# Optimization experiments

Measured on AMD Instinct MI355X. Metric: run time of the kernel, lower is better.

## Reference

```python
import jax, jax.numpy as jnp
import numpy as np
import math


def setup_inputs() -> dict:
    key = jax.random.key(0)
    k0, k1, k2, k3, k4 = jax.random.split(key, 5)
    in_f, out_f, nb = 512, 512, 8
    B, S = 4, 2048
    x = jax.random.normal(k0, (B, S, in_f), dtype=jnp.float32)
    # RBF params (frozen in original: basis_trainable=False)
    fan_in = in_f  # fan_in of rbf.weight.T which is (num_basis, in_features)
    bound = 1.0 / math.sqrt(fan_in)
    rbf_weight = jax.random.uniform(k1, (in_f, nb), dtype=jnp.float32,
                                    minval=-math.sqrt(3.0) * 0.33 / math.sqrt(fan_in),
                                    maxval=math.sqrt(3.0) * 0.33 / math.sqrt(fan_in))
    rbf_centers = jnp.tile(jnp.linspace(-bound, bound, nb, dtype=jnp.float32)[None, :], (in_f, 1))
    # KAN spline weight (in, nb, out); fan_in for init is in_f*nb
    fan2 = in_f * nb
    wb = math.sqrt(3.0) * 0.33 / math.sqrt(fan2)
    weight = jax.random.uniform(k2, (in_f, nb, out_f), dtype=jnp.float32, minval=-wb, maxval=wb)
    bias = jax.random.uniform(k3, (out_f,), dtype=jnp.float32,
                              minval=-1.0 / math.sqrt(fan2), maxval=1.0 / math.sqrt(fan2))
    scale_base = jax.random.uniform(k4, (in_f, out_f), dtype=jnp.float32, minval=-0.1, maxval=0.1)
    return {"x": x, "rbf_weight": rbf_weight, "rbf_centers": rbf_centers,
            "weight": weight, "bias": bias, "scale_base": scale_base}


def reference(x, rbf_weight, rbf_centers, weight, bias, scale_base):
    in_f = x.shape[-1]
    nb = rbf_weight.shape[1]
    beta = (nb / math.log2(nb)) ** 2  # get_rbf_width(2/nb, log2(nb))
    batch_shape = x.shape[:-1]
    xf = x.reshape(-1, in_f)  # (N, in)
    # RBF basis expansion: (N, in, nb)
    z = xf[:, :, None] * rbf_weight[None, :, :] - rbf_centers[None, :, :]
    phi = jnp.exp(-beta * (z * z))
    # spline contraction + base path, expressed as efficient contractions
    y = jnp.einsum('nib,ibo->no', phi, weight)
    y = y + bias + jnp.cos(xf) @ scale_base
    return y.reshape(*batch_shape, weight.shape[-1])
```

## Files before the change

kernel.cpp:

```cpp
#include <hip/hip_runtime.h>
#include <hip/hip_bf16.h>

typedef __attribute__((ext_vector_type(8))) short short8;
typedef __attribute__((ext_vector_type(4))) float f32x4;

#define IN_F 512
#define OUT_F 512
#define BK 64
#define PHI_STEPS 64
#define NSTEPS 72
#define PAN 64
#define ACH 512
#define BCH4 1024
#define NT4 4
#define BCH2 2048
#define NT2 2
#define PART_ELEMS (8192 * OUT_F)
#define C2 (-10.2591705f)

__device__ __forceinline__ short f2bf(float f) {
  unsigned u = __builtin_bit_cast(unsigned, f);
  u += 0x7fffu + ((u >> 16) & 1u);
  return (short)(u >> 16);
}

__device__ __forceinline__ void glds16(const void* g, void* l) {
  __builtin_amdgcn_global_load_lds(
      (const __attribute__((address_space(1))) unsigned int*)g,
      (__attribute__((address_space(3))) unsigned int*)l, 16, 0, 0);
}

__device__ __forceinline__ float bsrc(const float* __restrict__ w,
                                      const float* __restrict__ sb,
                                      int k, int col) {
  return (k < IN_F * 8) ? w[(size_t)k * OUT_F + col]
                        : sb[(size_t)(k - IN_F * 8) * OUT_F + col];
}

__global__ void __launch_bounds__(256) prep_b4(const float* __restrict__ w,
                                               const float* __restrict__ sb,
                                               short* __restrict__ img) {
  const int D = blockIdx.x * 256 + threadIdx.x;
  const int ci = D & (BCH4 - 1);
  const int im = D >> 10;
  const int s = im % NSTEPS;
  const int nt = im / NSTEPS;
  const int n = ci >> 3, slot = ci & 7;
  const int oct = slot ^ (n & 7);
  const int col = nt * 128 + n;
  short8 v;
#pragma unroll
  for (int j = 0; j < 8; ++j) v[j] = f2bf(bsrc(w, sb, s * 64 + oct * 8 + j, col));
  *(short8*)&img[(size_t)D * 8] = v;
}

__global__ void __launch_bounds__(256) prep_b2(const float* __restrict__ w,
                                               const float* __restrict__ sb,
                                               short* __restrict__ img) {
  const int D = blockIdx.x * 256 + threadIdx.x;
  const int ci = D & (BCH2 - 1);
  const int im = D >> 11;
  const int s = im % NSTEPS;
  const int nt = im / NSTEPS;
  const int n = ci >> 3, slot = ci & 7;
  const int oct = slot ^ (n & 7);
  const int col = nt * 256 + n;
  short8 v;
#pragma unroll
  for (int j = 0; j < 8; ++j) v[j] = f2bf(bsrc(w, sb, s * 64 + oct * 8 + j, col));
  *(short8*)&img[(size_t)D * 8] = v;
}

__global__ void __launch_bounds__(256) prep_a(const float* __restrict__ x,
                                              const float* __restrict__ rw,
                                              const float* __restrict__ rc,
                                              short* __restrict__ aimg) {
  const int D = blockIdx.x * 256 + threadIdx.x;
  const int ci = D & (ACH - 1);
  const int rest = D >> 9;
  const int s = rest % NSTEPS;
  const int pan = rest / NSTEPS;
  const int m = ci >> 3, slot = ci & 7;
  const int oct = slot ^ (m & 7);
  const int row = pan * PAN + m;
  short8 v;
  if (s < PHI_STEPS) {
    const int feat = s * 8 + oct;
    const float xv = x[(size_t)row * IN_F + feat];
    const float4 r0 = *(const float4*)(rw + feat * 8);
    const float4 r1 = *(const float4*)(rw + feat * 8 + 4);
    const float4 q0 = *(const float4*)(rc + feat * 8);
    const float4 q1 = *(const float4*)(rc + feat * 8 + 4);
    const float rwv[8] = {r0.x, r0.y, r0.z, r0.w, r1.x, r1.y, r1.z, r1.w};
    const float rcv[8] = {q0.x, q0.y, q0.z, q0.w, q1.x, q1.y, q1.z, q1.w};
#pragma unroll
    for (int j = 0; j < 8; ++j) {
      const float z = fmaf(xv, rwv[j], -rcv[j]);
      v[j] = f2bf(exp2f(C2 * z * z));
    }
  } else {
    const float* xp = x + (size_t)row * IN_F + (s - PHI_STEPS) * 64 + oct * 8;
    const float4 u0 = *(const float4*)xp, u1 = *(const float4*)(xp + 4);
    v[0] = f2bf(__cosf(u0.x)); v[1] = f2bf(__cosf(u0.y));
    v[2] = f2bf(__cosf(u0.z)); v[3] = f2bf(__cosf(u0.w));
    v[4] = f2bf(__cosf(u1.x)); v[5] = f2bf(__cosf(u1.y));
    v[6] = f2bf(__cosf(u1.z)); v[7] = f2bf(__cosf(u1.w));
  }
  *(short8*)&aimg[(size_t)D * 8] = v;
}

__global__ void __launch_bounds__(256) reduce_add(const float* __restrict__ part,
                                                  float* __restrict__ out) {
  const int n4 = PART_ELEMS / 4;
  const float4* p4 = (const float4*)part;
  float4* o4 = (float4*)out;
  for (int i = blockIdx.x * 256 + threadIdx.x; i < n4; i += gridDim.x * 256) {
    float4 a = o4[i];
    const float4 b = p4[i];
    a.x += b.x; a.y += b.y; a.z += b.z; a.w += b.w;
    o4[i] = a;
  }
}

template <int KS>
__global__ void __launch_bounds__(256, 2) kan_gemm(
    const short* __restrict__ aimg, const short* __restrict__ bimg,
    const float* __restrict__ bias, float* __restrict__ out,
    float* __restrict__ part) {
  constexpr int SPLC = NSTEPS / KS;
  __shared__ __align__(16) short A_lds[2][128 * BK];
  __shared__ __align__(16) short B_lds[2][128 * BK];

  const int t = threadIdx.x, lane = t & 63, wid = t >> 6;
  const int wm = wid >> 1, wn = wid & 1;
  const int l15 = lane & 15, kb = lane >> 4;
  const int mb = blockIdx.x, nt = blockIdx.y;
  const int ks = (KS > 1) ? blockIdx.z : 0;
  const int m0 = mb * 128, n0 = nt * 128, s0 = ks * SPLC;

  f32x4 acc[4][4];
#pragma unroll
  for (int i = 0; i < 4; ++i)
#pragma unroll
    for (int j = 0; j < 4; ++j) acc[i][j] = (f32x4){0.f, 0.f, 0.f, 0.f};

  auto stage = [&](int s, int buf) {
#pragma unroll
    for (int c = 0; c < 4; ++c) {
      const int p = c >> 1;
      const short* src = aimg +
          (((size_t)(2 * mb + p) * NSTEPS + s) * ACH + (c & 1) * 256 + wid * 64 + lane) * 8;
      glds16(src, &A_lds[buf][c * 2048 + wid * 512]);
    }
#pragma unroll
    for (int c = 0; c < 4; ++c) {
      const short* src = bimg +
          (((size_t)nt * NSTEPS + s) * BCH4 + c * 256 + wid * 64 + lane) * 8;
      glds16(src, &B_lds[buf][c * 2048 + wid * 512]);
    }
  };

  auto mfma_step = [&](int buf) {
#pragma unroll
    for (int kk = 0; kk < 2; ++kk) {
      const int sk = kk * 4 + kb;
      short8 af[4], bf[4];
#pragma unroll
      for (int mi = 0; mi < 4; ++mi) {
        const int r = wm * 64 + mi * 16 + l15;
        af[mi] = *(const short8*)&A_lds[buf][r * BK + (sk ^ (r & 7)) * 8];
      }
#pragma unroll
      for (int ni = 0; ni < 4; ++ni) {
        const int n = wn * 64 + ni * 16 + l15;
        bf[ni] = *(const short8*)&B_lds[buf][n * BK + (sk ^ (n & 7)) * 8];
      }
#pragma unroll
      for (int mi = 0; mi < 4; ++mi)
#pragma unroll
        for (int ni = 0; ni < 4; ++ni)
          acc[mi][ni] = __builtin_amdgcn_mfma_f32_16x16x32_bf16(
              af[mi], bf[ni], acc[mi][ni], 0, 0, 0);
    }
  };

  stage(s0, 0);

  for (int si = 0; si < SPLC; ++si) {
    const int c = si & 1;
    if (si + 1 < SPLC) {
      stage(s0 + si + 1, c ^ 1);
      asm volatile("s_waitcnt vmcnt(8)" ::: "memory");
    } else {
      asm volatile("s_waitcnt vmcnt(0)" ::: "memory");
    }
    __builtin_amdgcn_s_barrier();
    mfma_step(c);
    __builtin_amdgcn_s_barrier();
  }

#pragma unroll
  for (int ni = 0; ni < 4; ++ni) {
    const int col = n0 + wn * 64 + ni * 16 + l15;
    const float bb = (KS == 1 || ks == 0) ? bias[col] : 0.f;
#pragma unroll
    for (int mi = 0; mi < 4; ++mi) {
      const int rb = m0 + wm * 64 + mi * 16 + kb * 4;
#pragma unroll
      for (int r4 = 0; r4 < 4; ++r4) {
        const size_t idx = (size_t)(rb + r4) * OUT_F + col;
        if (KS == 1 || ks == 0) out[idx] = acc[mi][ni][r4] + bb;
        else                    part[idx] = acc[mi][ni][r4];
      }
    }
  }
}

template <int KS>
__global__ void __launch_bounds__(256, 2) kan_fused(
    const float* __restrict__ x, const float* __restrict__ rw,
    const float* __restrict__ rc, const float* __restrict__ bias,
    const short* __restrict__ bimg, float* __restrict__ out,
    float* __restrict__ part) {
  constexpr int SPLC = NSTEPS / KS;
  __shared__ __align__(16) short A_lds[2][64 * BK];
  __shared__ __align__(16) short B_lds[2][256 * BK];

  const int t = threadIdx.x, lane = t & 63, wid = t >> 6;
  const int l15 = lane & 15, kb = lane >> 4;
  const int m0 = blockIdx.x * 64;
  const int nt = blockIdx.y, n0 = nt * 256;
  const int ks = (KS > 1) ? blockIdx.z : 0;
  const int s0 = ks * SPLC;
  const int a_il = t & 7, a_m = t >> 3;

  f32x4 acc[4][4];
#pragma unroll
  for (int i = 0; i < 4; ++i)
#pragma unroll
    for (int j = 0; j < 4; ++j) acc[i][j] = (f32x4){0.f, 0.f, 0.f, 0.f};

  float xrA, xrB;
  float4 pr0, pr1, pc0, pc1, cA0, cA1, cB0, cB1;

  auto loadNext = [&](int s1) {
    if (s1 < PHI_STEPS) {
      const int feat = s1 * 8 + a_il;
      xrA = x[(size_t)(m0 + a_m) * IN_F + feat];
      xrB = x[(size_t)(m0 + a_m + 32) * IN_F + feat];
      pr0 = *(const float4*)(rw + feat * 8);
      pr1 = *(const float4*)(rw + feat * 8 + 4);
      pc0 = *(const float4*)(rc + feat * 8);
      pc1 = *(const float4*)(rc + feat * 8 + 4);
    } else {
      const float* xpA = x + (size_t)(m0 + a_m) * IN_F + (s1 - PHI_STEPS) * 64 + a_il * 8;
      const float* xpB = xpA + (size_t)32 * IN_F;
      cA0 = *(const float4*)xpA; cA1 = *(const float4*)(xpA + 4);
      cB0 = *(const float4*)xpB; cB1 = *(const float4*)(xpB + 4);
    }
  };

  auto writeA = [&](int s1, short* __restrict__ Ad) {
    short8 avA, avB;
    if (s1 < PHI_STEPS) {
      const float rwv[8] = {pr0.x, pr0.y, pr0.z, pr0.w, pr1.x, pr1.y, pr1.z, pr1.w};
      const float rcv[8] = {pc0.x, pc0.y, pc0.z, pc0.w, pc1.x, pc1.y, pc1.z, pc1.w};
#pragma unroll
      for (int b = 0; b < 8; ++b) {
        const float zA = fmaf(xrA, rwv[b], -rcv[b]);
        const float zB = fmaf(xrB, rwv[b], -rcv[b]);
        avA[b] = f2bf(exp2f(C2 * zA * zA));
        avB[b] = f2bf(exp2f(C2 * zB * zB));
      }
    } else {
      avA[0] = f2bf(__cosf(cA0.x)); avA[1] = f2bf(__cosf(cA0.y));
      avA[2] = f2bf(__cosf(cA0.z)); avA[3] = f2bf(__cosf(cA0.w));
      avA[4] = f2bf(__cosf(cA1.x)); avA[5] = f2bf(__cosf(cA1.y));
      avA[6] = f2bf(__cosf(cA1.z)); avA[7] = f2bf(__cosf(cA1.w));
      avB[0] = f2bf(__cosf(cB0.x)); avB[1] = f2bf(__cosf(cB0.y));
      avB[2] = f2bf(__cosf(cB0.z)); avB[3] = f2bf(__cosf(cB0.w));
      avB[4] = f2bf(__cosf(cB1.x)); avB[5] = f2bf(__cosf(cB1.y));
      avB[6] = f2bf(__cosf(cB1.z)); avB[7] = f2bf(__cosf(cB1.w));
    }
    const int mA = a_m, mB = a_m + 32;
    *(short8*)&Ad[mA * BK + (a_il ^ (mA & 7)) * 8] = avA;
    *(short8*)&Ad[mB * BK + (a_il ^ (mB & 7)) * 8] = avB;
  };

  auto stageB = [&](int s, short* __restrict__ Bd) {
    const short* src = bimg + ((size_t)(nt * NSTEPS + s) * BCH2 + t) * 8;
#pragma unroll
    for (int c = 0; c < 8; ++c)
      glds16(src + (size_t)c * 256 * 8, Bd + c * 2048 + wid * 512);
  };

  auto mfma_half = [&](const short* __restrict__ Ab, const short* __restrict__ Bb,
                       int kk) {
    const int sk = kk * 4 + kb;
    short8 af[4], bf[4];
#pragma unroll
    for (int mi = 0; mi < 4; ++mi) {
      const int r = mi * 16 + l15;
      af[mi] = *(const short8*)&Ab[r * BK + (sk ^ (r & 7)) * 8];
    }
#pragma unroll
    for (int ni = 0; ni < 4; ++ni) {
      const int n = wid * 64 + ni * 16 + l15;
      bf[ni] = *(const short8*)&Bb[n * BK + (sk ^ (n & 7)) * 8];
    }
#pragma unroll
    for (int mi = 0; mi < 4; ++mi)
#pragma unroll
      for (int ni = 0; ni < 4; ++ni)
        acc[mi][ni] = __builtin_amdgcn_mfma_f32_16x16x32_bf16(
            af[mi], bf[ni], acc[mi][ni], 0, 0, 0);
  };

  stageB(s0, B_lds[0]);
  loadNext(s0);
  writeA(s0, A_lds[0]);
  __syncthreads();

  for (int si = 0; si < SPLC; ++si) {
    const int c = si & 1;
    const int s = s0 + si;
    if (si + 1 < SPLC) { stageB(s + 1, B_lds[c ^ 1]); loadNext(s + 1); }
    mfma_half(A_lds[c], B_lds[c], 0);
    if (si + 1 < SPLC) writeA(s + 1, A_lds[c ^ 1]);
    mfma_half(A_lds[c], B_lds[c], 1);
    __syncthreads();
  }

#pragma unroll
  for (int ni = 0; ni < 4; ++ni) {
    const int col = n0 + wid * 64 + ni * 16 + l15;
    const float bb = (KS == 1 || ks == 0) ? bias[col] : 0.f;
#pragma unroll
    for (int mi = 0; mi < 4; ++mi) {
      const int rb = m0 + mi * 16 + kb * 4;
#pragma unroll
      for (int r4 = 0; r4 < 4; ++r4) {
        const size_t idx = (size_t)(rb + r4) * OUT_F + col;
        if (KS == 1 || ks == 0) out[idx] = acc[mi][ni][r4] + bb;
        else                    part[idx] = acc[mi][ni][r4];
      }
    }
  }
}

extern "C" void kernel_launch(void* const* d_in, const int* in_sizes, int n_in,
                              void* d_out, int out_size, void* d_ws, size_t ws_size,
                              hipStream_t stream) {
  const float* x    = (const float*)d_in[0];
  const float* rw   = (const float*)d_in[1];
  const float* rc   = (const float*)d_in[2];
  const float* w    = (const float*)d_in[3];
  const float* bias = (const float*)d_in[4];
  const float* sb   = (const float*)d_in[5];
  float* out = (float*)d_out;

  const int nrows = in_sizes[0] / IN_F;
  const int npan = nrows / PAN;

  const size_t b4_bytes   = (size_t)NT4 * NSTEPS * BCH4 * 16;
  const size_t b2_bytes   = (size_t)NT2 * NSTEPS * BCH2 * 16;
  const size_t aimg_bytes = (size_t)npan * NSTEPS * ACH * 16;
  const size_t part_bytes = (size_t)PART_ELEMS * sizeof(float);

  if (ws_size >= b4_bytes + aimg_bytes + part_bytes) {
    short* bimg = (short*)d_ws;
    short* aimg = (short*)((char*)d_ws + b4_bytes);
    float* part = (float*)((char*)d_ws + b4_bytes + aimg_bytes);
    prep_b4<<<NT4 * NSTEPS * BCH4 / 256, 256, 0, stream>>>(w, sb, bimg);
    prep_a<<<npan * NSTEPS * ACH / 256, 256, 0, stream>>>(x, rw, rc, aimg);
    kan_gemm<2><<<dim3(nrows / 128, 4, 2), 256, 0, stream>>>(aimg, bimg, bias, out, part);
    reduce_add<<<2048, 256, 0, stream>>>(part, out);
  } else if (ws_size >= b4_bytes + aimg_bytes) {
    short* bimg = (short*)d_ws;
    short* aimg = (short*)((char*)d_ws + b4_bytes);
    prep_b4<<<NT4 * NSTEPS * BCH4 / 256, 256, 0, stream>>>(w, sb, bimg);
    prep_a<<<npan * NSTEPS * ACH / 256, 256, 0, stream>>>(x, rw, rc, aimg);
    kan_gemm<1><<<dim3(nrows / 128, 4, 1), 256, 0, stream>>>(aimg, bimg, bias, out, nullptr);
  } else if (ws_size >= b2_bytes + part_bytes) {
    short* bimg = (short*)d_ws;
    float* part = (float*)((char*)d_ws + b2_bytes);
    prep_b2<<<NT2 * NSTEPS * BCH2 / 256, 256, 0, stream>>>(w, sb, bimg);
    kan_fused<2><<<dim3(nrows / 64, NT2, 2), 256, 0, stream>>>(x, rw, rc, bias,
                                                               bimg, out, part);
    reduce_add<<<2048, 256, 0, stream>>>(part, out);
  } else {
    short* bimg = (short*)d_ws;
    prep_b2<<<NT2 * NSTEPS * BCH2 / 256, 256, 0, stream>>>(w, sb, bimg);
    kan_fused<1><<<dim3(nrows / 64, NT2, 1), 256, 0, stream>>>(x, rw, rc, bias,
                                                               bimg, out, nullptr);
  }
}
```

Baseline: 83.28 us.

## Drop split-K GEMM, use 512-thread blocks with 4-stage LDS pipeline

Removes the split-K path and its partial-buffer write plus reduce_add kernel. The GEMM now runs 512-thread blocks (8 waves, each computing a 64x32 sub-tile) over all 72 K steps, with a 4-deep LDS prefetch ring instead of double buffering. This removes the extra reduction traffic and one launch, at the cost of halving grid parallelism (256 blocks) and using 128KB of LDS per block, which may limit occupancy to one block per CU.

```diff
diff --git a/kernel.cpp b/kernel.cpp
--- a/kernel.cpp
+++ b/kernel.cpp
@@ -122,75 +122,74 @@
   }
 }
 
-template <int KS>
-__global__ void __launch_bounds__(256, 2) kan_gemm(
+__global__ void __launch_bounds__(512, 2) kan_gemm(
     const short* __restrict__ aimg, const short* __restrict__ bimg,
-    const float* __restrict__ bias, float* __restrict__ out,
-    float* __restrict__ part) {
-  constexpr int SPLC = NSTEPS / KS;
-  __shared__ __align__(16) short A_lds[2][128 * BK];
-  __shared__ __align__(16) short B_lds[2][128 * BK];
+    const float* __restrict__ bias, float* __restrict__ out) {
+  __shared__ __align__(16) short A_lds[4][128 * BK];
+  __shared__ __align__(16) short B_lds[4][128 * BK];
 
   const int t = threadIdx.x, lane = t & 63, wid = t >> 6;
-  const int wm = wid >> 1, wn = wid & 1;
+  const int wm = wid >> 2, wn = wid & 3;
   const int l15 = lane & 15, kb = lane >> 4;
   const int mb = blockIdx.x, nt = blockIdx.y;
-  const int ks = (KS > 1) ? blockIdx.z : 0;
-  const int m0 = mb * 128, n0 = nt * 128, s0 = ks * SPLC;
-
-  f32x4 acc[4][4];
+  const int m0 = mb * 128, n0 = nt * 128;
+
+  f32x4 acc[4][2];
 #pragma unroll
   for (int i = 0; i < 4; ++i)
 #pragma unroll
-    for (int j = 0; j < 4; ++j) acc[i][j] = (f32x4){0.f, 0.f, 0.f, 0.f};
+    for (int j = 0; j < 2; ++j) acc[i][j] = (f32x4){0.f, 0.f, 0.f, 0.f};
+
+  const short* ab0 = aimg + (size_t)(2 * mb) * NSTEPS * ACH * 8;
+  const short* ab1 = aimg + (size_t)(2 * mb + 1) * NSTEPS * ACH * 8;
+  const short* bb = bimg + (size_t)nt * NSTEPS * BCH4 * 8;
 
   auto stage = [&](int s, int buf) {
-#pragma unroll
-    for (int c = 0; c < 4; ++c) {
-      const int p = c >> 1;
-      const short* src = aimg +
-          (((size_t)(2 * mb + p) * NSTEPS + s) * ACH + (c & 1) * 256 + wid * 64 + lane) * 8;
-      glds16(src, &A_lds[buf][c * 2048 + wid * 512]);
-    }
-#pragma unroll
-    for (int c = 0; c < 4; ++c) {
-      const short* src = bimg +
-          (((size_t)nt * NSTEPS + s) * BCH4 + c * 256 + wid * 64 + lane) * 8;
-      glds16(src, &B_lds[buf][c * 2048 + wid * 512]);
-    }
+    const size_t off = ((size_t)s * ACH + t) * 8;
+    glds16(ab0 + off, &A_lds[buf][wid * 512]);
+    glds16(ab1 + off, &A_lds[buf][4096 + wid * 512]);
+    const size_t boff = ((size_t)s * BCH4 + t) * 8;
+    glds16(bb + boff, &B_lds[buf][wid * 512]);
+    glds16(bb + boff + 512 * 8, &B_lds[buf][4096 + wid * 512]);
   };
 
   auto mfma_step = [&](int buf) {
 #pragma unroll
     for (int kk = 0; kk < 2; ++kk) {
       const int sk = kk * 4 + kb;
-      short8 af[4], bf[4];
+      short8 af[4], bf[2];
 #pragma unroll
       for (int mi = 0; mi < 4; ++mi) {
         const int r = wm * 64 + mi * 16 + l15;
         af[mi] = *(const short8*)&A_lds[buf][r * BK + (sk ^ (r & 7)) * 8];
       }
 #pragma unroll
-      for (int ni = 0; ni < 4; ++ni) {
-        const int n = wn * 64 + ni * 16 + l15;
+      for (int ni = 0; ni < 2; ++ni) {
+        const int n = wn * 32 + ni * 16 + l15;
         bf[ni] = *(const short8*)&B_lds[buf][n * BK + (sk ^ (n & 7)) * 8];
       }
 #pragma unroll
       for (int mi = 0; mi < 4; ++mi)
 #pragma unroll
-        for (int ni = 0; ni < 4; ++ni)
+        for (int ni = 0; ni < 2; ++ni)
           acc[mi][ni] = __builtin_amdgcn_mfma_f32_16x16x32_bf16(
               af[mi], bf[ni], acc[mi][ni], 0, 0, 0);
     }
   };
 
-  stage(s0, 0);
-
-  for (int si = 0; si < SPLC; ++si) {
-    const int c = si & 1;
-    if (si + 1 < SPLC) {
-      stage(s0 + si + 1, c ^ 1);
+  stage(0, 0);
+  stage(1, 1);
+  stage(2, 2);
+
+  for (int si = 0; si < NSTEPS; ++si) {
+    const int c = si & 3;
+    if (si + 3 < NSTEPS) {
+      stage(si + 3, (si + 3) & 3);
+      asm volatile("s_waitcnt vmcnt(12)" ::: "memory");
+    } else if (si + 2 < NSTEPS) {
       asm volatile("s_waitcnt vmcnt(8)" ::: "memory");
+    } else if (si + 1 < NSTEPS) {
+      asm volatile("s_waitcnt vmcnt(4)" ::: "memory");
     } else {
       asm volatile("s_waitcnt vmcnt(0)" ::: "memory");
     }
@@ -200,18 +199,15 @@
   }
 
 #pragma unroll
-  for (int ni = 0; ni < 4; ++ni) {
-    const int col = n0 + wn * 64 + ni * 16 + l15;
-    const float bb = (KS == 1 || ks == 0) ? bias[col] : 0.f;
+  for (int ni = 0; ni < 2; ++ni) {
+    const int col = n0 + wn * 32 + ni * 16 + l15;
+    const float bb_ = bias[col];
 #pragma unroll
     for (int mi = 0; mi < 4; ++mi) {
       const int rb = m0 + wm * 64 + mi * 16 + kb * 4;
 #pragma unroll
-      for (int r4 = 0; r4 < 4; ++r4) {
-        const size_t idx = (size_t)(rb + r4) * OUT_F + col;
-        if (KS == 1 || ks == 0) out[idx] = acc[mi][ni][r4] + bb;
-        else                    part[idx] = acc[mi][ni][r4];
-      }
+      for (int r4 = 0; r4 < 4; ++r4)
+        out[(size_t)(rb + r4) * OUT_F + col] = acc[mi][ni][r4] + bb_;
     }
   }
 }
@@ -367,20 +363,12 @@
   const size_t aimg_bytes = (size_t)npan * NSTEPS * ACH * 16;
   const size_t part_bytes = (size_t)PART_ELEMS * sizeof(float);
 
-  if (ws_size >= b4_bytes + aimg_bytes + part_bytes) {
-    short* bimg = (short*)d_ws;
-    short* aimg = (short*)((char*)d_ws + b4_bytes);
-    float* part = (float*)((char*)d_ws + b4_bytes + aimg_bytes);
-    prep_b4<<<NT4 * NSTEPS * BCH4 / 256, 256, 0, stream>>>(w, sb, bimg);
-    prep_a<<<npan * NSTEPS * ACH / 256, 256, 0, stream>>>(x, rw, rc, aimg);
-    kan_gemm<2><<<dim3(nrows / 128, 4, 2), 256, 0, stream>>>(aimg, bimg, bias, out, part);
-    reduce_add<<<2048, 256, 0, stream>>>(part, out);
-  } else if (ws_size >= b4_bytes + aimg_bytes) {
+  if (ws_size >= b4_bytes + aimg_bytes) {
     short* bimg = (short*)d_ws;
     short* aimg = (short*)((char*)d_ws + b4_bytes);
     prep_b4<<<NT4 * NSTEPS * BCH4 / 256, 256, 0, stream>>>(w, sb, bimg);
     prep_a<<<npan * NSTEPS * ACH / 256, 256, 0, stream>>>(x, rw, rc, aimg);
-    kan_gemm<1><<<dim3(nrows / 128, 4, 1), 256, 0, stream>>>(aimg, bimg, bias, out, nullptr);
+    kan_gemm<<<dim3(nrows / 128, 4), 512, 0, stream>>>(aimg, bimg, bias, out);
   } else if (ws_size >= b2_bytes + part_bytes) {
     short* bimg = (short*)d_ws;
     float* part = (float*)((char*)d_ws + b2_bytes);
```

Result: slower. 96.28 us (+15.6%).
